# Performance work log

Measured on AMD Instinct MI355X. Metric: run time of the kernel, lower is better.

Reference implementation:

```python
import jax, jax.numpy as jnp
import numpy as np

IN_CHANNELS = 64
OUT_CHANNELS = 64
SEQ_LEN = 512
KERNEL_SIZE = 9
STRIDE = 1
PADDING = 4  # symmetric
OUT_SEQ_LEN = (SEQ_LEN + 2 * PADDING - (KERNEL_SIZE - 1) - 1) // STRIDE + 1  # 512


def setup_inputs() -> dict:
    key = jax.random.key(0)
    k1, k2, k3 = jax.random.split(key, 3)
    x = jax.random.normal(k1, (64, IN_CHANNELS, SEQ_LEN), dtype=jnp.float32)
    # nn.init.normal_(std=0.1)
    weight = 0.1 * jax.random.normal(k2, (IN_CHANNELS, OUT_CHANNELS, KERNEL_SIZE, OUT_SEQ_LEN), dtype=jnp.float32)
    bias = 0.1 * jax.random.normal(k3, (OUT_CHANNELS, OUT_SEQ_LEN), dtype=jnp.float32)
    return {"x": x, "weight": weight, "bias": bias}


def reference(x, weight, bias):
    # x: [B, Ci, S] -> pad last dim
    xp = jnp.pad(x, ((0, 0), (0, 0), (PADDING, PADDING)))
    # Unfold (im2col) as a gather: same math as the one-hot grouped conv.
    starts = jnp.arange(OUT_SEQ_LEN) * STRIDE            # [L]
    offs = jnp.arange(KERNEL_SIZE)                        # [K]
    idx = starts[:, None] + offs[None, :]                 # [L, K]
    patches = xp[:, :, idx]                               # [B, Ci, L, K]
    # per-position matmul: 'b i l k, i o k l -> b o l'
    out = jnp.einsum('bilk,iokl->bol', patches, weight)
    out = out + bias                                      # [B, Co, L]
    return out
```

## Files before the change

### kernel.cpp

```cpp
#include <hip/hip_runtime.h>


#define CIN   64
#define COUT  64
#define SEQ   512
#define KS    9
#define LT    8
#define OT    16
#define LWIN  16
#define XSTR  72
#define XLW   (64*XSTR)
#define BOS   40
#define BLS   (OT*BOS + 8)
#define NSTEP 18
#define WSTR  (COUT*KS*SEQ)
#define XS_ELEMS (LWIN*XLW)
#define BS_ELEMS (LT*BLS)
#define LDS_BYTES ((XS_ELEMS + BS_ELEMS)*2)

typedef __attribute__((ext_vector_type(8))) short bf16x8;
typedef __attribute__((ext_vector_type(4))) float f32x4;

__device__ __forceinline__ ushort f2bf(float f) {
    return (ushort)((__float_as_uint(f) + 0x8000u) >> 16);
}
__device__ __forceinline__ uint pack2bf(float a0, float a1) {
    uint u0 = __float_as_uint(a0) + 0x8000u;
    uint u1 = __float_as_uint(a1) + 0x8000u;
    return __builtin_amdgcn_perm(u1, u0, 0x07060302);
}

__global__ __launch_bounds__(1024, 4)
void lc1d_mfma(const float* __restrict__ x, const float* __restrict__ w,
               const float* __restrict__ bias, float* __restrict__ out)
{
    extern __shared__ ushort lds[];
    ushort* Xs = lds;
    ushort* Bs = lds + XS_ELEMS;

    const int tid  = threadIdx.x;
    const int lane = tid & 63;
    const int wv   = tid >> 6;
    const int lt = blockIdx.x >> 2;
    const int os = blockIdx.x & 3;
    const int l0 = lt * LT;
    const int o0 = os * OT;

    const int lh = tid & 1;
    const int oo = (tid >> 1) & 15;
    const int ip = (tid >> 5) & 15;
    const bool stager = (tid < 512);

    const float* wbase = w + ((size_t)(2*ip) * COUT + (o0 + oo)) * (KS*SEQ)
                           + l0 + lh*4;
    float4 pfA[2], pfB[2];

    #define LOAD_STEP(pf, c) if (stager) {                                       \
        const int k_ = (c) >> 1, ih_ = (c) & 1;                                  \
        const float* p_ = wbase + (size_t)(ih_*32) * WSTR + (size_t)k_ * SEQ;    \
        pf[0] = *(const float4*)p_;                                              \
        pf[1] = *(const float4*)(p_ + WSTR);                                     \
    }

    #define WRITE_BS(pf) if (stager) {                                           \
        _Pragma("unroll")                                                        \
        for (int dl = 0; dl < 4; ++dl) {                                         \
            uint pk = pack2bf((&pf[0].x)[dl], (&pf[1].x)[dl]);                   \
            *(uint*)(Bs + (lh*4+dl)*BLS + oo*BOS + 2*ip) = pk;                   \
        }                                                                        \
    }

    LOAD_STEP(pfA, 0)
    LOAD_STEP(pfB, 1)

    #pragma unroll
    for (int it = 0; it < 16; ++it) {
        int flat = tid + 1024*it;
        int row = flat >> 2;
        int q   = flat & 3;
        int b = row >> 6, i = row & 63;
        const float* src = x + ((size_t)(b*CIN + i))*SEQ + (l0 - 4) + q*4;
        float4 v = make_float4(0.f, 0.f, 0.f, 0.f);
        if (!((lt == 0 && q == 0) || (lt == 63 && q == 3)))
            v = *(const float4*)src;
        ushort* dst = Xs + (q*4)*XLW + b*XSTR + i;
        dst[0*XLW] = f2bf(v.x);
        dst[1*XLW] = f2bf(v.y);
        dst[2*XLW] = f2bf(v.z);
        dst[3*XLW] = f2bf(v.w);
    }

    f32x4 acc[2];
    acc[0] = (f32x4)0.0f;
    acc[1] = (f32x4)0.0f;

    const int lrel = wv & 7;
    const int btb  = (wv >> 3) * 2;
    const int am   = (lane & 15) * XSTR + (lane >> 4) * 8;
    const int boff = lrel*BLS + (lane & 15) * BOS + (lane >> 4) * 8;

    __syncthreads();

    #define DO_MFMA(c) {                                                         \
        const int k_ = (c) >> 1, ih_ = (c) & 1;                                  \
        bf16x8 Bf = *(const bf16x8*)(Bs + boff);                                 \
        const ushort* Arow = Xs + (lrel + k_)*XLW + ih_*32 + am;                 \
        _Pragma("unroll")                                                        \
        for (int jt = 0; jt < 2; ++jt) {                                         \
            bf16x8 Af = *(const bf16x8*)(Arow + (btb + jt)*(16*XSTR));           \
            acc[jt] = __builtin_amdgcn_mfma_f32_16x16x32_bf16(Af, Bf, acc[jt],   \
                                                              0, 0, 0);          \
        }                                                                        \
    }

    for (int cc = 0; cc < NSTEP; cc += 2) {
        WRITE_BS(pfA)
        __syncthreads();
        if (cc + 2 < NSTEP) LOAD_STEP(pfA, cc + 2)
        DO_MFMA(cc)
        __syncthreads();

        WRITE_BS(pfB)
        __syncthreads();
        if (cc + 3 < NSTEP) LOAD_STEP(pfB, cc + 3)
        DO_MFMA(cc + 1)
        __syncthreads();
    }

    const int l    = l0 + lrel;
    const int orow = o0 + (lane & 15);
    const int rbase = (lane >> 4) * 4;
    const float bv = bias[orow*SEQ + l];
    #pragma unroll
    for (int jt = 0; jt < 2; ++jt) {
        #pragma unroll
        for (int r = 0; r < 4; ++r) {
            const int b = (btb + jt)*16 + rbase + r;
            out[((size_t)(b*COUT + orow))*SEQ + l] = acc[jt][r] + bv;
        }
    }
}

extern "C" void kernel_launch(void* const* d_in, const int* in_sizes, int n_in,
                              void* d_out, int out_size, void* d_ws, size_t ws_size,
                              hipStream_t stream) {
    const float* x    = (const float*)d_in[0];
    const float* wgt  = (const float*)d_in[1];
    const float* bias = (const float*)d_in[2];
    float* out        = (float*)d_out;

    hipFuncSetAttribute((const void*)lc1d_mfma,
                        hipFuncAttributeMaxDynamicSharedMemorySize, LDS_BYTES);
    dim3 grid(256);
    lc1d_mfma<<<grid, 1024, LDS_BYTES, stream>>>(x, wgt, bias, out);
}
```

Before: 152.5 us.

## Retile locally-connected conv to 16 positions x 8 outputs with ring-buffered weight prefetch

Changes each block's tile from 8 sequence positions x 16 output channels to 16 positions x 8 channels. The 16-wide MFMA N dimension is padded by feeding zeros from LDS to the upper 8 lanes. Weight loads move to a 3-deep register ring with double-buffered LDS slots, which cuts syncs to one per step. X is staged per input half as packed bf16 pairs, with the second half reloaded mid-loop. The aim is to raise x reuse and cut barriers, at the cost of half the MFMA work being wasted on zero padding.

After: 134.1 us. -12.1%, faster.

```diff
diff --git a/kernel.cpp b/kernel.cpp
--- a/kernel.cpp
+++ b/kernel.cpp
@@ -5,25 +5,24 @@
 #define COUT  64
 #define SEQ   512
 #define KS    9
-#define LT    8
-#define OT    16
-#define LWIN  16
-#define XSTR  72
-#define XLW   (64*XSTR)
+#define LT    16
+#define OT    8
+#define LWIN  24
+#define WSTR  (COUT*KS*SEQ)
+#define XBS   40
+#define XLW   (64*XBS)
+#define XS_ELEMS (LWIN*XLW)
 #define BOS   40
 #define BLS   (OT*BOS + 8)
+#define BSLOT (LT*BLS)
+#define ZOFF  (XS_ELEMS + 2*BSLOT)
+#define LDS_USH (ZOFF + 64)
+#define LDS_BYTES (LDS_USH*2)
 #define NSTEP 18
-#define WSTR  (COUT*KS*SEQ)
-#define XS_ELEMS (LWIN*XLW)
-#define BS_ELEMS (LT*BLS)
-#define LDS_BYTES ((XS_ELEMS + BS_ELEMS)*2)
 
 typedef __attribute__((ext_vector_type(8))) short bf16x8;
 typedef __attribute__((ext_vector_type(4))) float f32x4;
 
-__device__ __forceinline__ ushort f2bf(float f) {
-    return (ushort)((__float_as_uint(f) + 0x8000u) >> 16);
-}
 __device__ __forceinline__ uint pack2bf(float a0, float a1) {
     uint u0 = __float_as_uint(a0) + 0x8000u;
     uint u1 = __float_as_uint(a1) + 0x8000u;
@@ -36,107 +35,127 @@
 {
     extern __shared__ ushort lds[];
     ushort* Xs = lds;
-    ushort* Bs = lds + XS_ELEMS;
+    ushort* BsB = lds + XS_ELEMS;
 
     const int tid  = threadIdx.x;
     const int lane = tid & 63;
-    const int wv   = tid >> 6;
-    const int lt = blockIdx.x >> 2;
-    const int os = blockIdx.x & 3;
+    const int wvid = tid >> 6;
+    const int bt = wvid & 3;
+    const int lg = wvid >> 2;
+    const int lt = blockIdx.x >> 3;
+    const int os = blockIdx.x & 7;
     const int l0 = lt * LT;
     const int o0 = os * OT;
 
-    const int lh = tid & 1;
-    const int oo = (tid >> 1) & 15;
-    const int ip = (tid >> 5) & 15;
     const bool stager = (tid < 512);
+    const int lf  = tid & 3;
+    const int oo  = (tid >> 2) & 7;
+    const int ipp = (tid >> 5) & 15;
 
-    const float* wbase = w + ((size_t)(2*ip) * COUT + (o0 + oo)) * (KS*SEQ)
-                           + l0 + lh*4;
-    float4 pfA[2], pfB[2];
+    const float* wbase = w + ((size_t)(2*ipp)*COUT + (o0 + oo))*(KS*SEQ) + l0 + lf*4;
 
-    #define LOAD_STEP(pf, c) if (stager) {                                       \
-        const int k_ = (c) >> 1, ih_ = (c) & 1;                                  \
-        const float* p_ = wbase + (size_t)(ih_*32) * WSTR + (size_t)k_ * SEQ;    \
-        pf[0] = *(const float4*)p_;                                              \
-        pf[1] = *(const float4*)(p_ + WSTR);                                     \
+    float4 rA[3], rB[3];
+
+    #define LOAD_RING(sl, s) if (stager && (s) < NSTEP) {                        \
+        const int ih_ = (s) / 9, k_ = (s) - 9*ih_;                               \
+        const float* p_ = wbase + (size_t)ih_*32*WSTR + k_*SEQ;                  \
+        rA[sl] = *(const float4*)p_;                                             \
+        rB[sl] = *(const float4*)(p_ + WSTR);                                    \
     }
 
-    #define WRITE_BS(pf) if (stager) {                                           \
+    #define WRITE_BS(sl, s) if (stager) {                                        \
+        ushort* dst_ = BsB + ((s)&1)*BSLOT + oo*BOS + 2*ipp;                     \
         _Pragma("unroll")                                                        \
         for (int dl = 0; dl < 4; ++dl) {                                         \
-            uint pk = pack2bf((&pf[0].x)[dl], (&pf[1].x)[dl]);                   \
-            *(uint*)(Bs + (lh*4+dl)*BLS + oo*BOS + 2*ip) = pk;                   \
+            uint pk_ = pack2bf((&rA[sl].x)[dl], (&rB[sl].x)[dl]);                \
+            *(uint*)(dst_ + (lf*4+dl)*BLS) = pk_;                                \
         }                                                                        \
     }
 
-    LOAD_STEP(pfA, 0)
-    LOAD_STEP(pfB, 1)
-
-    #pragma unroll
-    for (int it = 0; it < 16; ++it) {
-        int flat = tid + 1024*it;
-        int row = flat >> 2;
-        int q   = flat & 3;
-        int b = row >> 6, i = row & 63;
-        const float* src = x + ((size_t)(b*CIN + i))*SEQ + (l0 - 4) + q*4;
-        float4 v = make_float4(0.f, 0.f, 0.f, 0.f);
-        if (!((lt == 0 && q == 0) || (lt == 63 && q == 3)))
-            v = *(const float4*)src;
-        ushort* dst = Xs + (q*4)*XLW + b*XSTR + i;
-        dst[0*XLW] = f2bf(v.x);
-        dst[1*XLW] = f2bf(v.y);
-        dst[2*XLW] = f2bf(v.z);
-        dst[3*XLW] = f2bf(v.w);
+    #define STAGE_XS(ih) {                                                       \
+        const int qq  = tid & 7;                                                 \
+        const int rp0 = tid >> 3;                                                \
+        if (qq < 6) {                                                            \
+            _Pragma("unroll")                                                    \
+            for (int it = 0; it < 8; ++it) {                                     \
+                const int rp = rp0 + it*128;                                     \
+                const int b_ = rp >> 4, ip_ = rp & 15;                           \
+                const float* s0 = x + ((size_t)(b_*CIN) + (ih)*32 + 2*ip_)*SEQ   \
+                                    + (l0 - 4) + qq*4;                           \
+                float4 v0 = make_float4(0.f,0.f,0.f,0.f), v1 = v0;               \
+                if (!((lt == 0 && qq == 0) || (lt == 31 && qq == 5))) {          \
+                    v0 = *(const float4*)s0;                                     \
+                    v1 = *(const float4*)(s0 + SEQ);                             \
+                }                                                                \
+                ushort* d_ = Xs + b_*XBS + 2*ip_;                                \
+                _Pragma("unroll")                                                \
+                for (int dl = 0; dl < 4; ++dl)                                   \
+                    *(uint*)(d_ + (qq*4+dl)*XLW) = pack2bf((&v0.x)[dl],          \
+                                                           (&v1.x)[dl]);         \
+            }                                                                    \
+        }                                                                        \
     }
 
-    f32x4 acc[2];
-    acc[0] = (f32x4)0.0f;
-    acc[1] = (f32x4)0.0f;
+    const int aoff = (bt*16 + (lane & 15))*XBS + (lane >> 4)*8;
+    const int boff = (lane & 15)*BOS + (lane >> 4)*8;
+    const bool nhi = (lane & 15) >= 8;
+    const ushort* zptr = lds + ZOFF + (lane >> 4)*8;
 
-    const int lrel = wv & 7;
-    const int btb  = (wv >> 3) * 2;
-    const int am   = (lane & 15) * XSTR + (lane >> 4) * 8;
-    const int boff = lrel*BLS + (lane & 15) * BOS + (lane >> 4) * 8;
+    f32x4 acc[4];
+    #pragma unroll
+    for (int j = 0; j < 4; ++j) acc[j] = (f32x4)0.0f;
 
-    __syncthreads();
-
-    #define DO_MFMA(c) {                                                         \
-        const int k_ = (c) >> 1, ih_ = (c) & 1;                                  \
-        bf16x8 Bf = *(const bf16x8*)(Bs + boff);                                 \
-        const ushort* Arow = Xs + (lrel + k_)*XLW + ih_*32 + am;                 \
+    #define DO_MFMA(s) {                                                         \
+        const int k_ = (s) % 9;                                                  \
+        const ushort* BsS = BsB + ((s)&1)*BSLOT;                                 \
         _Pragma("unroll")                                                        \
-        for (int jt = 0; jt < 2; ++jt) {                                         \
-            bf16x8 Af = *(const bf16x8*)(Arow + (btb + jt)*(16*XSTR));           \
-            acc[jt] = __builtin_amdgcn_mfma_f32_16x16x32_bf16(Af, Bf, acc[jt],   \
+        for (int dl = 0; dl < 4; ++dl) {                                         \
+            const int ll = lg*4 + dl;                                            \
+            bf16x8 Af = *(const bf16x8*)(Xs + (ll + k_)*XLW + aoff);             \
+            const ushort* Bp = nhi ? zptr : (BsS + ll*BLS + boff);               \
+            bf16x8 Bf = *(const bf16x8*)Bp;                                      \
+            acc[dl] = __builtin_amdgcn_mfma_f32_16x16x32_bf16(Af, Bf, acc[dl],   \
                                                               0, 0, 0);          \
         }                                                                        \
     }
 
-    for (int cc = 0; cc < NSTEP; cc += 2) {
-        WRITE_BS(pfA)
-        __syncthreads();
-        if (cc + 2 < NSTEP) LOAD_STEP(pfA, cc + 2)
-        DO_MFMA(cc)
-        __syncthreads();
-
-        WRITE_BS(pfB)
-        __syncthreads();
-        if (cc + 3 < NSTEP) LOAD_STEP(pfB, cc + 3)
-        DO_MFMA(cc + 1)
-        __syncthreads();
+    #define STEP(s) {                                                            \
+        if ((s) < NSTEP-1) WRITE_BS(((s)+1)%3, (s)+1)                            \
+        LOAD_RING(((s)+1)%3, (s)+4)                                              \
+        DO_MFMA(s)                                                               \
+        __syncthreads();                                                         \
     }
 
-    const int l    = l0 + lrel;
-    const int orow = o0 + (lane & 15);
-    const int rbase = (lane >> 4) * 4;
-    const float bv = bias[orow*SEQ + l];
-    #pragma unroll
-    for (int jt = 0; jt < 2; ++jt) {
+    LOAD_RING(0, 0)
+    LOAD_RING(1, 1)
+    LOAD_RING(2, 2)
+    if (tid < 64) lds[ZOFF + tid] = 0;
+    STAGE_XS(0)
+    WRITE_BS(0, 0)
+    LOAD_RING(0, 3)
+    __syncthreads();
+
+    STEP(0)  STEP(1)  STEP(2)  STEP(3)  STEP(4)
+    STEP(5)  STEP(6)  STEP(7)  STEP(8)
+
+    STAGE_XS(1)
+    __syncthreads();
+
+    STEP(9)  STEP(10) STEP(11) STEP(12) STEP(13)
+    STEP(14) STEP(15) STEP(16) STEP(17)
+
+    if (!nhi) {
+        const int og = o0 + (lane & 15);
+        const int rb = (lane >> 4)*4;
         #pragma unroll
-        for (int r = 0; r < 4; ++r) {
-            const int b = (btb + jt)*16 + rbase + r;
-            out[((size_t)(b*COUT + orow))*SEQ + l] = acc[jt][r] + bv;
+        for (int dl = 0; dl < 4; ++dl) {
+            const int lgl = l0 + lg*4 + dl;
+            const float bv = bias[og*SEQ + lgl];
+            #pragma unroll
+            for (int r = 0; r < 4; ++r) {
+                const int bg = bt*16 + rb + r;
+                out[((size_t)(bg*COUT + og))*SEQ + lgl] = acc[dl][r] + bv;
+            }
         }
     }
 }
```
